# Optimization experiments

Hardware: AMD Instinct MI355X
Metric: run time of the kernel (lower is better)

## Reference

```python
import jax, jax.numpy as jnp
import numpy as np

N = 1_000_000   # memory slots (current_size == memory_size)
D = 64          # embedding_dim == compressed_dim (required by the source code)
B = 64          # query batch
QBITS = 8       # quantization_bits


def setup_inputs() -> dict:
    key = jax.random.key(0)
    ks = jax.random.split(key, 6)
    return {
        "query": jax.random.normal(ks[0], (B, D), dtype=jnp.float32),
        "memory": jax.random.normal(ks[1], (N, D), dtype=jnp.float32),
        "attention_weights": jax.random.normal(ks[2], (N,), dtype=jnp.float32),
        "Wq": jax.random.normal(ks[3], (D, D), dtype=jnp.float32) / np.sqrt(D),
        "Wk": jax.random.normal(ks[4], (D, D), dtype=jnp.float32) / np.sqrt(D),
        "Wv": jax.random.normal(ks[5], (D, D), dtype=jnp.float32) / np.sqrt(D),
        "top_k": 5,
    }


def reference(query, memory, attention_weights, Wq, Wk, Wv, top_k):
    d = memory.shape[1]
    levels = jnp.float32(2 ** QBITS - 1)
    # _quantize_tensor / _dequantize_tensor round-trip on the stored memory
    mn = memory.min()
    mx = memory.max()
    scale = (mx - mn) / levels
    zero_point = -mn / scale
    mem_dq = (jnp.round(memory / scale + zero_point) - zero_point) * scale  # [N, D]

    q = query @ Wq.T                    # [B, D]
    keys = mem_dq @ Wk.T                # [N, D]
    values = mem_dq @ Wv.T              # [N, D]

    # attention scores + per-slot bias
    scores = q @ keys.T / np.float32(np.sqrt(d)) + attention_weights[None, :]  # [B, N]

    top_scores, top_idx = jax.lax.top_k(scores, top_k)   # [B, k]
    gathered = jnp.take(values, top_idx, axis=0)         # [B, k, D] irregular gather
    dist = jax.nn.softmax(top_scores, axis=-1)           # [B, k]
    out = jnp.einsum('bk,bkd->bd', dist, gathered)       # [B, D]
    return out
```

## Files before the change

kernel.cpp:

```cpp
#include <hip/hip_runtime.h>
#include <stdint.h>

constexpr int NROWS = 1000000;
constexpr int D = 64;
constexpr int B = 64;
constexpr int TOPK = 5;
constexpr int TBLK = 4;
constexpr int TRES = 16;
constexpr int NB2MAX = 1024;

typedef __attribute__((ext_vector_type(8))) short short8;
typedef __attribute__((ext_vector_type(4))) float floatx4;
typedef unsigned long long u64;

#define OFF_QKF   512
#define OFF_QKB   16896
#define OFF_MM    25088
#define OFF_CAND  57856

__device__ __forceinline__ unsigned fkey(float x) {
    unsigned u = __float_as_uint(x);
    return (u & 0x80000000u) ? ~u : (u | 0x80000000u);
}
__device__ __forceinline__ float fkey_inv(unsigned k) {
    unsigned u = (k & 0x80000000u) ? (k ^ 0x80000000u) : ~k;
    return __uint_as_float(u);
}
__device__ __forceinline__ unsigned short f2bf_rne(float x) {
    unsigned u = __float_as_uint(x);
    u += 0x7fffu + ((u >> 16) & 1u);
    return (unsigned short)(u >> 16);
}

template<int K>
__device__ __forceinline__ void insert_key(u64 (&ks)[K], u64 key) {
    if (key > ks[K - 1]) {
        #pragma unroll
        for (int j = K - 1; j > 0; --j)
            ks[j] = (key > ks[j - 1]) ? ks[j - 1] : ((key > ks[j]) ? key : ks[j]);
        ks[0] = (key > ks[0]) ? key : ks[0];
    }
}

__device__ __forceinline__ void insert2(u64& a, u64& b, u64 key) {
    u64 hi = key > a ? key : a;
    u64 lo = key > a ? a : key;
    b = lo > b ? lo : b;
    a = hi;
}

__global__ void k_qk(const float* __restrict__ query, const float* __restrict__ Wq,
                     const float* __restrict__ Wk,
                     float* __restrict__ qkf, unsigned short* __restrict__ qkb) {
    __shared__ float q[4][64];
    int t = threadIdx.x;
    int b0 = blockIdx.x * 4;
    int bq = t >> 6, d = t & 63;
    float s1 = 0.f;
    for (int e = 0; e < 64; e++) s1 += query[(b0 + bq) * 64 + e] * Wq[d * 64 + e];
    q[bq][d] = s1;
    __syncthreads();
    float v = 0.f;
    for (int dd = 0; dd < 64; dd++) v += q[bq][dd] * Wk[dd * 64 + d];
    v *= 0.125f;
    qkf[(b0 + bq) * 64 + d] = v;
    qkb[(b0 + bq) * 64 + d] = f2bf_rne(v);
}

__launch_bounds__(256, 4)
__global__ void k_score_mm(const float* __restrict__ mem, const float* __restrict__ aw,
                           const unsigned short* __restrict__ qkb,
                           u64* __restrict__ cand,
                           unsigned* __restrict__ part, int wrows) {
    __shared__ u64 mrg[4][4][16][2];
    __shared__ float swmn[4], swmx[4];

    int t = threadIdx.x;
    int l15 = t & 15, quad = (t >> 4) & 3, w = t >> 6;

    short8 bq[4][2];
    #pragma unroll
    for (int bt = 0; bt < 4; bt++) {
        #pragma unroll
        for (int kb = 0; kb < 2; kb++)
            bq[bt][kb] = *(const short8*)(qkb + (bt * 16 + l15) * 64 + kb * 32 + quad * 8);
    }

    u64 Ltop[4], Lsec[4];
    #pragma unroll
    for (int bt = 0; bt < 4; bt++) { Ltop[bt] = 0ull; Lsec[bt] = 0ull; }

    float mnv = 3.402823466e38f, mxv = -3.402823466e38f;

    int gw = blockIdx.x * 4 + w;
    int wbeg = gw * wrows;
    int wend = min(wbeg + wrows, NROWS);
    int span = wend - wbeg;
    int nt = span > 0 ? (span >> 4) : 0;

    const char* pbase = (const char*)mem + (size_t)wbeg * 256 + (size_t)(l15 * 256 + quad * 32);
    const float* abase = aw + wbeg + quad * 4;

    float4 p0, p1, p2, p3, pa;
    if (nt > 0) {
        p0 = *(const float4*)(pbase);
        p1 = *(const float4*)(pbase + 16);
        p2 = *(const float4*)(pbase + 128);
        p3 = *(const float4*)(pbase + 144);
        pa = *(const float4*)(abase);
    }

    for (int it = 0; it < nt; ++it) {
        float4 c0 = p0, c1 = p1, c2 = p2, c3 = p3;
        float aw0 = pa.x, aw1 = pa.y, aw2 = pa.z, aw3 = pa.w;

        int nx = (it + 1 < nt) ? (it + 1) : (nt - 1);
        const char* pn = pbase + (size_t)nx * 4096;
        p0 = *(const float4*)(pn);
        p1 = *(const float4*)(pn + 16);
        p2 = *(const float4*)(pn + 128);
        p3 = *(const float4*)(pn + 144);
        pa = *(const float4*)(abase + nx * 16);

        mnv = fminf(mnv, fminf(fminf(c0.x, c0.y), fminf(c0.z, c0.w)));
        mxv = fmaxf(mxv, fmaxf(fmaxf(c0.x, c0.y), fmaxf(c0.z, c0.w)));
        mnv = fminf(mnv, fminf(fminf(c1.x, c1.y), fminf(c1.z, c1.w)));
        mxv = fmaxf(mxv, fmaxf(fmaxf(c1.x, c1.y), fmaxf(c1.z, c1.w)));
        mnv = fminf(mnv, fminf(fminf(c2.x, c2.y), fminf(c2.z, c2.w)));
        mxv = fmaxf(mxv, fmaxf(fmaxf(c2.x, c2.y), fmaxf(c2.z, c2.w)));
        mnv = fminf(mnv, fminf(fminf(c3.x, c3.y), fminf(c3.z, c3.w)));
        mxv = fmaxf(mxv, fmaxf(fmaxf(c3.x, c3.y), fmaxf(c3.z, c3.w)));

        short8 a0, a1;
        a0[0] = (short)f2bf_rne(c0.x); a0[1] = (short)f2bf_rne(c0.y);
        a0[2] = (short)f2bf_rne(c0.z); a0[3] = (short)f2bf_rne(c0.w);
        a0[4] = (short)f2bf_rne(c1.x); a0[5] = (short)f2bf_rne(c1.y);
        a0[6] = (short)f2bf_rne(c1.z); a0[7] = (short)f2bf_rne(c1.w);
        a1[0] = (short)f2bf_rne(c2.x); a1[1] = (short)f2bf_rne(c2.y);
        a1[2] = (short)f2bf_rne(c2.z); a1[3] = (short)f2bf_rne(c2.w);
        a1[4] = (short)f2bf_rne(c3.x); a1[5] = (short)f2bf_rne(c3.y);
        a1[6] = (short)f2bf_rne(c3.z); a1[7] = (short)f2bf_rne(c3.w);

        int gr = wbeg + it * 16 + quad * 4;

        #pragma unroll
        for (int bt = 0; bt < 4; bt++) {
            floatx4 acc = {aw0, aw1, aw2, aw3};
            acc = __builtin_amdgcn_mfma_f32_16x16x32_bf16(a0, bq[bt][0], acc, 0, 0, 0);
            acc = __builtin_amdgcn_mfma_f32_16x16x32_bf16(a1, bq[bt][1], acc, 0, 0, 0);
            #pragma unroll
            for (int r = 0; r < 4; r++) {
                u64 key = ((u64)fkey(acc[r]) << 32) | (unsigned)(~(unsigned)(gr + r));
                insert2(Ltop[bt], Lsec[bt], key);
            }
        }
    }

    #pragma unroll
    for (int o = 32; o > 0; o >>= 1) {
        mnv = fminf(mnv, __shfl_xor(mnv, o));
        mxv = fmaxf(mxv, __shfl_xor(mxv, o));
    }
    if ((t & 63) == 0) { swmn[w] = mnv; swmx[w] = mxv; }

    #pragma unroll
    for (int bt = 0; bt < 4; bt++) {
        #pragma unroll
        for (int dlt = 16; dlt <= 32; dlt <<= 1) {
            u64 ka = __shfl_xor(Ltop[bt], dlt);
            u64 kb = __shfl_xor(Lsec[bt], dlt);
            insert2(Ltop[bt], Lsec[bt], ka);
            insert2(Ltop[bt], Lsec[bt], kb);
        }
    }
    if ((t & 48) == 0) {
        #pragma unroll
        for (int bt = 0; bt < 4; bt++) {
            mrg[w][bt][l15][0] = Ltop[bt];
            mrg[w][bt][l15][1] = Lsec[bt];
        }
    }
    __syncthreads();

    if (t == 0) {
        float a = fminf(fminf(swmn[0], swmn[1]), fminf(swmn[2], swmn[3]));
        float b2 = fmaxf(fmaxf(swmx[0], swmx[1]), fmaxf(swmx[2], swmx[3]));
        part[blockIdx.x * 2 + 0] = fkey(a);
        part[blockIdx.x * 2 + 1] = fkey(b2);
    }
    if (t < 64) {
        u64 ts[TBLK];
        #pragma unroll
        for (int j = 0; j < TBLK; j++) ts[j] = 0ull;
        int bt = t >> 4, l = t & 15;
        #pragma unroll
        for (int w2 = 0; w2 < 4; w2++) {
            insert_key<TBLK>(ts, mrg[w2][bt][l][0]);
            insert_key<TBLK>(ts, mrg[w2][bt][l][1]);
        }
        #pragma unroll
        for (int j = 0; j < TBLK; j++)
            cand[((long long)blockIdx.x * 64 + t) * TBLK + j] = ts[j];
    }
}

__global__ void k_finalize(const u64* __restrict__ cand, int nb2,
                           const float* __restrict__ mem, const float* __restrict__ aw,
                           const float* __restrict__ Wv, const unsigned* __restrict__ part,
                           const float* __restrict__ qkf, float* __restrict__ out) {
    __shared__ u64 lists[256][TRES];
    __shared__ float qkr[64];
    __shared__ int exid[TRES];
    __shared__ u64 exkey[TRES];
    __shared__ float exsc[TRES];
    __shared__ float wsel[TOPK];
    __shared__ int isel[TOPK];
    __shared__ float su[64];
    __shared__ unsigned redmn[4], redmx[4];
    __shared__ float sscale[2];

    int t = threadIdx.x, b = blockIdx.x;
    int total = nb2 * TBLK;

    unsigned mnk = 0xFFFFFFFFu, mxk = 0u;
    for (int i = t; i < nb2; i += 256) {
        unsigned a = part[2 * i], c = part[2 * i + 1];
        mnk = a < mnk ? a : mnk;
        mxk = c > mxk ? c : mxk;
    }
    #pragma unroll
    for (int o = 32; o > 0; o >>= 1) {
        unsigned am = __shfl_xor(mnk, o); mnk = am < mnk ? am : mnk;
        unsigned ax = __shfl_xor(mxk, o); mxk = ax > mxk ? ax : mxk;
    }
    int w4 = t >> 6;
    if ((t & 63) == 0) { redmn[w4] = mnk; redmx[w4] = mxk; }

    u64 loc[TRES];
    #pragma unroll
    for (int j = 0; j < TRES; j++) loc[j] = 0ull;
    for (int i = t; i < total; i += 256) {
        int blk = i / TBLK, j = i - blk * TBLK;
        insert_key<TRES>(loc, cand[((long long)blk * 64 + b) * TBLK + j]);
    }
    #pragma unroll
    for (int j = 0; j < TRES; j++) lists[t][j] = loc[j];
    if (t < 64) qkr[t] = qkf[b * 64 + t];
    __syncthreads();

    if (t == 255) {
        unsigned m0 = redmn[0], M0 = redmx[0];
        #pragma unroll
        for (int i = 1; i < 4; i++) {
            m0 = redmn[i] < m0 ? redmn[i] : m0;
            M0 = redmx[i] > M0 ? redmx[i] : M0;
        }
        float mnv = fkey_inv(m0), mxv = fkey_inv(M0);
        float scale = (mxv - mnv) / 255.0f;
        sscale[0] = scale;
        sscale[1] = -mnv / scale;
    }

    for (int s = 128; s > 0; s >>= 1) {
        if (t < s) {
            #pragma unroll
            for (int j = 0; j < TRES; j++) insert_key<TRES>(loc, lists[t + s][j]);
            #pragma unroll
            for (int j = 0; j < TRES; j++) lists[t][j] = loc[j];
        }
        __syncthreads();
    }
    if (t < TRES) {
        u64 k = lists[0][t];
        exid[t] = k ? (int)(~(unsigned)k) : 0;
    }
    __syncthreads();

    float scale = sscale[0], zp = sscale[1];

    int lane = t & 63, w = t >> 6;
    for (int i = 0; i < 4; i++) {
        int c = w * 4 + i;
        int idx = exid[c];
        float m = mem[(long long)idx * 64 + lane];
        float dq = (rintf(m / scale + zp) - zp) * scale;
        float p2 = dq * qkr[lane];
        for (int o = 32; o > 0; o >>= 1) p2 += __shfl_xor(p2, o);
        if (lane == 0) {
            float ex = p2 + aw[idx];
            exsc[c] = ex;
            exkey[c] = ((u64)fkey(ex) << 32) | (unsigned)(~(unsigned)idx);
        }
    }
    __syncthreads();

    if (t == 0) {
        u64 bnd = ~0ull;
        float ssel[TOPK];
        for (int p = 0; p < TOPK; p++) {
            u64 best = 0ull; int bc = 0;
            for (int c = 0; c < TRES; c++) {
                u64 k = exkey[c];
                if (k < bnd && k > best) { best = k; bc = c; }
            }
            bnd = best;
            ssel[p] = exsc[bc];
            isel[p] = exid[bc];
        }
        float Z = 0.f;
        for (int p = 0; p < TOPK; p++) { wsel[p] = expf(ssel[p] - ssel[0]); Z += wsel[p]; }
        for (int p = 0; p < TOPK; p++) wsel[p] /= Z;
    }
    __syncthreads();

    if (t < 64) {
        float u = 0.f;
        #pragma unroll
        for (int p = 0; p < TOPK; p++) {
            float m = mem[(long long)isel[p] * 64 + t];
            float dq = (rintf(m / scale + zp) - zp) * scale;
            u += wsel[p] * dq;
        }
        su[t] = u;
    }
    __syncthreads();
    if (t < 64) {
        float o = 0.f;
        #pragma unroll
        for (int e = 0; e < 64; e++) o += su[e] * Wv[t * 64 + e];
        out[b * 64 + t] = o;
    }
}

extern "C" void kernel_launch(void* const* d_in, const int* in_sizes, int n_in,
                              void* d_out, int out_size, void* d_ws, size_t ws_size,
                              hipStream_t stream) {
    const float* query = (const float*)d_in[0];
    const float* mem   = (const float*)d_in[1];
    const float* aw    = (const float*)d_in[2];
    const float* Wq    = (const float*)d_in[3];
    const float* Wk    = (const float*)d_in[4];
    const float* Wv    = (const float*)d_in[5];
    float* out = (float*)d_out;

    char* ws = (char*)d_ws;
    float* qkf     = (float*)(ws + OFF_QKF);
    unsigned short* qkb = (unsigned short*)(ws + OFF_QKB);
    unsigned* part = (unsigned*)(ws + OFF_MM);
    u64* cand = (u64*)(ws + OFF_CAND);

    int nb2 = NB2MAX;
    size_t need = (size_t)OFF_CAND + (size_t)nb2 * 64 * TBLK * 8;
    if (ws_size < need) {
        size_t avail = ws_size > OFF_CAND ? ws_size - OFF_CAND : 0;
        nb2 = (int)(avail / ((size_t)64 * TBLK * 8));
        if (nb2 < 8) nb2 = 8;
        if (nb2 > NB2MAX) nb2 = NB2MAX;
    }
    int waves = nb2 * 4;
    int wrows = ((NROWS + waves - 1) / waves + 15) / 16 * 16;

    k_qk<<<16, 256, 0, stream>>>(query, Wq, Wk, qkf, qkb);
    k_score_mm<<<nb2, 256, 0, stream>>>(mem, aw, qkb, cand, part, wrows);
    k_finalize<<<B, 256, 0, stream>>>(cand, nb2, mem, aw, Wv, part, qkf, out);
}
```

Measured before the change: 415.1 us.

## Pack score and local row into 32-bit keys and triple-buffer tile loads

The per-lane top-2 tracking moves from 64-bit keys to 32-bit keys. Each key holds the top 20 bits of the order-preserving score and a 12-bit row offset local to the wave, and is expanded back to 64-bit keys before the block merge. The attention-weight load becomes one scalar per lane, redistributed with shuffles. The single-stage prefetch becomes a three-deep rotating register buffer that keeps more memory loads in flight. Truncating the score key to 20 bits can change tie-breaking between near-equal scores, which candidate refinement must absorb, and the 12-bit offset assumes each wave covers at most 4096 rows.

```diff
diff --git a/kernel.cpp b/kernel.cpp
--- a/kernel.cpp
+++ b/kernel.cpp
@@ -42,11 +42,17 @@
     }
 }
 
-__device__ __forceinline__ void insert2(u64& a, u64& b, u64 key) {
-    u64 hi = key > a ? key : a;
-    u64 lo = key > a ? a : key;
+__device__ __forceinline__ void insert2u(unsigned& a, unsigned& b, unsigned key) {
+    unsigned hi = key > a ? key : a;
+    unsigned lo = key > a ? a : key;
     b = lo > b ? lo : b;
     a = hi;
+}
+
+__device__ __forceinline__ u64 expand_key(unsigned k32, int wbeg) {
+    if (!k32) return 0ull;
+    unsigned row = (unsigned)wbeg + (0xFFFu - (k32 & 0xFFFu));
+    return ((u64)(k32 & 0xFFFFF000u) << 32) | (unsigned)~row;
 }
 
 __global__ void k_qk(const float* __restrict__ query, const float* __restrict__ Wq,
@@ -77,6 +83,7 @@
 
     int t = threadIdx.x;
     int l15 = t & 15, quad = (t >> 4) & 3, w = t >> 6;
+    int qr = quad * 4;
 
     short8 bq[4][2];
     #pragma unroll
@@ -86,9 +93,9 @@
             bq[bt][kb] = *(const short8*)(qkb + (bt * 16 + l15) * 64 + kb * 32 + quad * 8);
     }
 
-    u64 Ltop[4], Lsec[4];
-    #pragma unroll
-    for (int bt = 0; bt < 4; bt++) { Ltop[bt] = 0ull; Lsec[bt] = 0ull; }
+    unsigned Ltop[4], Lsec[4];
+    #pragma unroll
+    for (int bt = 0; bt < 4; bt++) { Ltop[bt] = 0u; Lsec[bt] = 0u; }
 
     float mnv = 3.402823466e38f, mxv = -3.402823466e38f;
 
@@ -99,62 +106,73 @@
     int nt = span > 0 ? (span >> 4) : 0;
 
     const char* pbase = (const char*)mem + (size_t)wbeg * 256 + (size_t)(l15 * 256 + quad * 32);
-    const float* abase = aw + wbeg + quad * 4;
-
-    float4 p0, p1, p2, p3, pa;
+    const float* abase = aw + wbeg + (t & 15);
+
+    float4 A0, A1, A2, A3, B0, B1, B2, B3, C0, C1, C2, C3;
+    float aA = 0.f, aB = 0.f, aC = 0.f;
+
+#define LOADT(T0, T1, T2, T3, TA, TILE) do {                                   \
+        const char* pn_ = pbase + (size_t)(TILE) * 4096;                       \
+        T0 = *(const float4*)(pn_);                                            \
+        T1 = *(const float4*)(pn_ + 16);                                       \
+        T2 = *(const float4*)(pn_ + 128);                                      \
+        T3 = *(const float4*)(pn_ + 144);                                      \
+        TA = abase[(TILE) * 16];                                               \
+    } while (0)
+
+#define PROC(T0, T1, T2, T3, TA, IT) do {                                      \
+    mnv = fminf(mnv, fminf(fminf(T0.x, T0.y), fminf(T0.z, T0.w)));             \
+    mxv = fmaxf(mxv, fmaxf(fmaxf(T0.x, T0.y), fmaxf(T0.z, T0.w)));             \
+    mnv = fminf(mnv, fminf(fminf(T1.x, T1.y), fminf(T1.z, T1.w)));             \
+    mxv = fmaxf(mxv, fmaxf(fmaxf(T1.x, T1.y), fmaxf(T1.z, T1.w)));             \
+    mnv = fminf(mnv, fminf(fminf(T2.x, T2.y), fminf(T2.z, T2.w)));             \
+    mxv = fmaxf(mxv, fmaxf(fmaxf(T2.x, T2.y), fmaxf(T2.z, T2.w)));             \
+    mnv = fminf(mnv, fminf(fminf(T3.x, T3.y), fminf(T3.z, T3.w)));             \
+    mxv = fmaxf(mxv, fmaxf(fmaxf(T3.x, T3.y), fmaxf(T3.z, T3.w)));             \
+    short8 a0_, a1_;                                                           \
+    a0_[0] = (short)f2bf_rne(T0.x); a0_[1] = (short)f2bf_rne(T0.y);            \
+    a0_[2] = (short)f2bf_rne(T0.z); a0_[3] = (short)f2bf_rne(T0.w);            \
+    a0_[4] = (short)f2bf_rne(T1.x); a0_[5] = (short)f2bf_rne(T1.y);            \
+    a0_[6] = (short)f2bf_rne(T1.z); a0_[7] = (short)f2bf_rne(T1.w);            \
+    a1_[0] = (short)f2bf_rne(T2.x); a1_[1] = (short)f2bf_rne(T2.y);            \
+    a1_[2] = (short)f2bf_rne(T2.z); a1_[3] = (short)f2bf_rne(T2.w);            \
+    a1_[4] = (short)f2bf_rne(T3.x); a1_[5] = (short)f2bf_rne(T3.y);            \
+    a1_[6] = (short)f2bf_rne(T3.z); a1_[7] = (short)f2bf_rne(T3.w);            \
+    float aw0_ = __shfl(TA, qr);     float aw1_ = __shfl(TA, qr + 1);          \
+    float aw2_ = __shfl(TA, qr + 2); float aw3_ = __shfl(TA, qr + 3);          \
+    int idb_ = 0xFFF - (IT) * 16 - qr;                                         \
+    _Pragma("unroll")                                                          \
+    for (int bt_ = 0; bt_ < 4; bt_++) {                                        \
+        floatx4 acc_ = {aw0_, aw1_, aw2_, aw3_};                               \
+        acc_ = __builtin_amdgcn_mfma_f32_16x16x32_bf16(a0_, bq[bt_][0], acc_, 0, 0, 0); \
+        acc_ = __builtin_amdgcn_mfma_f32_16x16x32_bf16(a1_, bq[bt_][1], acc_, 0, 0, 0); \
+        _Pragma("unroll")                                                      \
+        for (int r_ = 0; r_ < 4; r_++) {                                       \
+            unsigned k_ = (fkey(acc_[r_]) & 0xFFFFF000u) | (unsigned)(idb_ - r_); \
+            insert2u(Ltop[bt_], Lsec[bt_], k_);                                \
+        }                                                                      \
+    }                                                                          \
+} while (0)
+
     if (nt > 0) {
-        p0 = *(const float4*)(pbase);
-        p1 = *(const float4*)(pbase + 16);
-        p2 = *(const float4*)(pbase + 128);
-        p3 = *(const float4*)(pbase + 144);
-        pa = *(const float4*)(abase);
-    }
-
-    for (int it = 0; it < nt; ++it) {
-        float4 c0 = p0, c1 = p1, c2 = p2, c3 = p3;
-        float aw0 = pa.x, aw1 = pa.y, aw2 = pa.z, aw3 = pa.w;
-
-        int nx = (it + 1 < nt) ? (it + 1) : (nt - 1);
-        const char* pn = pbase + (size_t)nx * 4096;
-        p0 = *(const float4*)(pn);
-        p1 = *(const float4*)(pn + 16);
-        p2 = *(const float4*)(pn + 128);
-        p3 = *(const float4*)(pn + 144);
-        pa = *(const float4*)(abase + nx * 16);
-
-        mnv = fminf(mnv, fminf(fminf(c0.x, c0.y), fminf(c0.z, c0.w)));
-        mxv = fmaxf(mxv, fmaxf(fmaxf(c0.x, c0.y), fmaxf(c0.z, c0.w)));
-        mnv = fminf(mnv, fminf(fminf(c1.x, c1.y), fminf(c1.z, c1.w)));
-        mxv = fmaxf(mxv, fmaxf(fmaxf(c1.x, c1.y), fmaxf(c1.z, c1.w)));
-        mnv = fminf(mnv, fminf(fminf(c2.x, c2.y), fminf(c2.z, c2.w)));
-        mxv = fmaxf(mxv, fmaxf(fmaxf(c2.x, c2.y), fmaxf(c2.z, c2.w)));
-        mnv = fminf(mnv, fminf(fminf(c3.x, c3.y), fminf(c3.z, c3.w)));
-        mxv = fmaxf(mxv, fmaxf(fmaxf(c3.x, c3.y), fmaxf(c3.z, c3.w)));
-
-        short8 a0, a1;
-        a0[0] = (short)f2bf_rne(c0.x); a0[1] = (short)f2bf_rne(c0.y);
-        a0[2] = (short)f2bf_rne(c0.z); a0[3] = (short)f2bf_rne(c0.w);
-        a0[4] = (short)f2bf_rne(c1.x); a0[5] = (short)f2bf_rne(c1.y);
-        a0[6] = (short)f2bf_rne(c1.z); a0[7] = (short)f2bf_rne(c1.w);
-        a1[0] = (short)f2bf_rne(c2.x); a1[1] = (short)f2bf_rne(c2.y);
-        a1[2] = (short)f2bf_rne(c2.z); a1[3] = (short)f2bf_rne(c2.w);
-        a1[4] = (short)f2bf_rne(c3.x); a1[5] = (short)f2bf_rne(c3.y);
-        a1[6] = (short)f2bf_rne(c3.z); a1[7] = (short)f2bf_rne(c3.w);
-
-        int gr = wbeg + it * 16 + quad * 4;
-
-        #pragma unroll
-        for (int bt = 0; bt < 4; bt++) {
-            floatx4 acc = {aw0, aw1, aw2, aw3};
-            acc = __builtin_amdgcn_mfma_f32_16x16x32_bf16(a0, bq[bt][0], acc, 0, 0, 0);
-            acc = __builtin_amdgcn_mfma_f32_16x16x32_bf16(a1, bq[bt][1], acc, 0, 0, 0);
-            #pragma unroll
-            for (int r = 0; r < 4; r++) {
-                u64 key = ((u64)fkey(acc[r]) << 32) | (unsigned)(~(unsigned)(gr + r));
-                insert2(Ltop[bt], Lsec[bt], key);
-            }
-        }
-    }
+        LOADT(A0, A1, A2, A3, aA, 0);
+        LOADT(B0, B1, B2, B3, aB, min(1, nt - 1));
+        LOADT(C0, C1, C2, C3, aC, min(2, nt - 1));
+    }
+    int it = 0;
+    for (; it + 3 <= nt; it += 3) {
+        PROC(A0, A1, A2, A3, aA, it);
+        LOADT(A0, A1, A2, A3, aA, min(it + 3, nt - 1));
+        PROC(B0, B1, B2, B3, aB, it + 1);
+        LOADT(B0, B1, B2, B3, aB, min(it + 4, nt - 1));
+        PROC(C0, C1, C2, C3, aC, it + 2);
+        LOADT(C0, C1, C2, C3, aC, min(it + 5, nt - 1));
+    }
+    if (it < nt)     PROC(A0, A1, A2, A3, aA, it);
+    if (it + 1 < nt) PROC(B0, B1, B2, B3, aB, it + 1);
+
+#undef LOADT
+#undef PROC
 
     #pragma unroll
     for (int o = 32; o > 0; o >>= 1) {
@@ -167,17 +185,17 @@
     for (int bt = 0; bt < 4; bt++) {
         #pragma unroll
         for (int dlt = 16; dlt <= 32; dlt <<= 1) {
-            u64 ka = __shfl_xor(Ltop[bt], dlt);
-            u64 kb = __shfl_xor(Lsec[bt], dlt);
-            insert2(Ltop[bt], Lsec[bt], ka);
-            insert2(Ltop[bt], Lsec[bt], kb);
+            unsigned ka = __shfl_xor(Ltop[bt], dlt);
+            unsigned kb = __shfl_xor(Lsec[bt], dlt);
+            insert2u(Ltop[bt], Lsec[bt], ka);
+            insert2u(Ltop[bt], Lsec[bt], kb);
         }
     }
     if ((t & 48) == 0) {
         #pragma unroll
         for (int bt = 0; bt < 4; bt++) {
-            mrg[w][bt][l15][0] = Ltop[bt];
-            mrg[w][bt][l15][1] = Lsec[bt];
+            mrg[w][bt][l15][0] = expand_key(Ltop[bt], wbeg);
+            mrg[w][bt][l15][1] = expand_key(Lsec[bt], wbeg);
         }
     }
     __syncthreads();
@@ -354,7 +372,7 @@
     if (ws_size < need) {
         size_t avail = ws_size > OFF_CAND ? ws_size - OFF_CAND : 0;
         nb2 = (int)(avail / ((size_t)64 * TBLK * 8));
-        if (nb2 < 8) nb2 = 8;
+        if (nb2 < 64) nb2 = 64;
         if (nb2 > NB2MAX) nb2 = NB2MAX;
     }
     int waves = nb2 * 4;
```

Result: slower. 445.9 us (+7.4%).
